# Performance work log

Hardware: AMD Instinct MI355X
Metric: run time of the kernel (lower is better)

Reference implementation:

```python
import jax, jax.numpy as jnp
from jax import lax
import numpy as np

B, H, W, C = 512, 64, 128, 3
FEAT = 13 * 26 * 64  # ceil(64/5)*ceil(128/5)*(32+32) after SAME stride-5 convs + concat


def setup_inputs() -> dict:
    key = jax.random.key(0)
    ks = jax.random.split(key, 6)
    x = jax.random.normal(ks[0], (B, H, W, C), jnp.float32)
    conv0_w = jax.random.normal(ks[1], (3, 3, 3, 32), jnp.float32) * 0.05  # HWIO
    conv1_w = jax.random.normal(ks[2], (5, 5, 3, 32), jnp.float32) * 0.05
    fc0_w = jax.random.normal(ks[3], (FEAT, 32), jnp.float32) * 0.01
    fc0_b = jnp.zeros((32,), jnp.float32)
    fc1_w = jax.random.normal(ks[4], (32, 6), jnp.float32) * 0.1
    fc1_b = jnp.zeros((6,), jnp.float32)
    return {"x": x, "conv0_w": conv0_w, "conv1_w": conv1_w,
            "fc0_w": fc0_w, "fc0_b": fc0_b, "fc1_w": fc1_w, "fc1_b": fc1_b}


def _stn_forward(x, conv0_w, conv1_w, fc0_w, fc0_b, fc1_w, fc1_b):
    b, h, w, c = x.shape
    dn = ("NHWC", "HWIO", "NHWC")
    # ---- LocNet ----
    # AveragePooling2D(3x3, stride 1, SAME); TF avg_pool averages over valid
    # (non-padded) elements only, so normalize by a window-count map.
    psum = lax.reduce_window(x, 0.0, lax.add, (1, 3, 3, 1), (1, 1, 1, 1), "SAME")
    cnt = lax.reduce_window(jnp.ones((1, h, w, 1), x.dtype), 0.0, lax.add,
                            (1, 3, 3, 1), (1, 1, 1, 1), "SAME")
    pooled = psum / cnt
    x0 = jax.nn.relu(lax.conv_general_dilated(pooled, conv0_w, (5, 5), "SAME",
                                              dimension_numbers=dn))
    x1 = jax.nn.relu(lax.conv_general_dilated(x, conv1_w, (5, 5), "SAME",
                                              dimension_numbers=dn))
    feat = jnp.concatenate([x0, x1], axis=-1).reshape(b, -1)
    # Dropout(0.5) is identity at inference.
    hid = jnp.tanh(feat @ fc0_w + fc0_b)
    theta = jnp.tanh(hid @ fc1_w + fc1_b).reshape(b, 2, 3)
    # ---- gen_grid ----
    xt, yt = jnp.meshgrid(jnp.linspace(-1.0, 1.0, w), jnp.linspace(-1.0, 1.0, h))
    grid = jnp.stack([xt.ravel(), yt.ravel(), jnp.ones(h * w, x.dtype)])  # [3, h*w]
    T = jnp.einsum("bij,jk->bik", theta, grid)          # [b, 2, h*w]
    T = T.reshape(b, 2, h, w).transpose(0, 2, 3, 1)     # [b, h, w, 2]
    # ---- grid_sample (bilinear) ----
    gx = (T[..., 0] + 1.0) * w / 2.0
    gy = (T[..., 1] + 1.0) * h / 2.0
    x0f = jnp.clip(jnp.floor(gx), 0.0, w - 2.0)
    x1f = jnp.clip(jnp.floor(gx) + 1.0, 1.0, w - 1.0)
    y0f = jnp.clip(jnp.floor(gy), 0.0, h - 2.0)
    y1f = jnp.clip(jnp.floor(gy) + 1.0, 1.0, h - 1.0)
    xi0, xi1 = x0f.astype(jnp.int32), x1f.astype(jnp.int32)
    yi0, yi1 = y0f.astype(jnp.int32), y1f.astype(jnp.int32)
    bi = jnp.arange(b)[:, None, None]                   # broadcast batch index
    Q00 = x[bi, yi0, xi0]  # [b, h, w, c]
    Q01 = x[bi, yi1, xi0]
    Q10 = x[bi, yi0, xi1]
    Q11 = x[bi, yi1, xi1]
    wx0 = (x1f - gx)[..., None]
    wx1 = (gx - x0f)[..., None]
    wy0 = (y1f - gy)[..., None]
    wy1 = (gy - y0f)[..., None]
    # Wx @ Q @ Wy expanded: rows of Q are x-neighbors, cols are y-neighbors.
    out = wx0 * (wy0 * Q00 + wy1 * Q01) + wx1 * (wy0 * Q10 + wy1 * Q11)
    Wd = ((x1f - x0f) * (y1f - y0f))[..., None]
    return out / Wd


def reference(x, conv0_w, conv1_w, fc0_w, fc0_b, fc1_w, fc1_b):
    return _stn_forward(x, conv0_w, conv1_w, fc0_w, fc0_b, fc1_w, fc1_b)
```

## Files before the change

kernel.cpp:

```cpp
#include <hip/hip_runtime.h>
#include <math.h>

namespace {
constexpr int BN = 512, HH = 64, WW = 128, CC = 3;
constexpr int OHH = 13, OWW = 26;
constexpr int FEATN = OHH * OWW * 64;
constexpr int KCH = 416;
constexpr int NKS = FEATN / KCH;
}

__global__ __launch_bounds__(256, 3) void k_feat(const float* __restrict__ x,
                                                 const float* __restrict__ w0,
                                                 const float* __restrict__ w1,
                                                 float* __restrict__ feat) {
  const int p = blockIdx.x * 256 + threadIdx.x;
  const int b = p / 338;
  const int pos = p - b * 338;
  const int oh = pos / 26;
  const int ow = pos - oh * 26;
  const float* xb = x + (size_t)b * (HH * WW * CC);

  float xv[6][15];
#pragma unroll
  for (int ri = 0; ri < 6; ++ri) {
    const int gr = oh * 5 - 1 + ri;
    const int grc = min(max(gr, 0), HH - 1);
    const bool rv = (gr >= 0) & (gr <= HH - 1);
    const float* rowp = xb + grc * (WW * CC);
#pragma unroll
    for (int pj = 0; pj < 5; ++pj) {
      const int gc = ow * 5 - 1 + pj;
      const int gcc = min(max(gc, 0), WW - 1);
      const bool v = rv & (gc >= 0) & (gc <= WW - 1);
      const float* pp = rowp + gcc * CC;
      const float f0 = pp[0], f1 = pp[1], f2 = pp[2];
      xv[ri][pj * 3 + 0] = v ? f0 : 0.f;
      xv[ri][pj * 3 + 1] = v ? f1 : 0.f;
      xv[ri][pj * 3 + 2] = v ? f2 : 0.f;
    }
  }

  float inv[3][3];
#pragma unroll
  for (int kh = 0; kh < 3; ++kh)
#pragma unroll
    for (int kw = 0; kw < 3; ++kw) {
      const int rc = 3 - ((oh == 0 && kh == 0) ? 1 : 0);
      int cc2 = 3;
      if (ow == 0 && kw == 0) cc2 = 2;
      if (ow == OWW - 1 && kw == 2) cc2 = 2;
      inv[kh][kw] = 1.0f / (float)(rc * cc2);
    }
  float pooled[27];
#pragma unroll
  for (int kh = 0; kh < 3; ++kh)
#pragma unroll
    for (int kw = 0; kw < 3; ++kw)
#pragma unroll
      for (int ic = 0; ic < 3; ++ic) {
        float s = 0.f;
#pragma unroll
        for (int dr = 0; dr < 3; ++dr)
#pragma unroll
          for (int dc = 0; dc < 3; ++dc)
            s += xv[kh + dr][(kw + dc) * 3 + ic];
        pooled[(kh * 3 + kw) * 3 + ic] = s * inv[kh][kw];
      }

  float* fb = feat + (size_t)p * 64;

#pragma unroll 1
  for (int qg = 0; qg < 8; ++qg) {
    float a0 = 0.f, a1 = 0.f, a2 = 0.f, a3 = 0.f;
#pragma unroll
    for (int tap = 0; tap < 27; ++tap) {
      const float pv = pooled[tap];
      const float4 wv = *(const float4*)(w0 + tap * 32 + qg * 4);
      a0 += pv * wv.x; a1 += pv * wv.y; a2 += pv * wv.z; a3 += pv * wv.w;
    }
    fb[qg * 4 + 0] = fmaxf(a0, 0.f);
    fb[qg * 4 + 1] = fmaxf(a1, 0.f);
    fb[qg * 4 + 2] = fmaxf(a2, 0.f);
    fb[qg * 4 + 3] = fmaxf(a3, 0.f);
  }

#pragma unroll 1
  for (int qg = 0; qg < 8; ++qg) {
    float a0 = 0.f, a1 = 0.f, a2 = 0.f, a3 = 0.f;
#pragma unroll
    for (int kh = 0; kh < 5; ++kh)
#pragma unroll
      for (int kw = 0; kw < 5; ++kw)
#pragma unroll
        for (int ic = 0; ic < 3; ++ic) {
          const float pv = xv[kh + 1][kw * 3 + ic];
          const int tap = (kh * 5 + kw) * 3 + ic;
          const float4 wv = *(const float4*)(w1 + tap * 32 + qg * 4);
          a0 += pv * wv.x; a1 += pv * wv.y; a2 += pv * wv.z; a3 += pv * wv.w;
        }
    fb[32 + qg * 4 + 0] = fmaxf(a0, 0.f);
    fb[32 + qg * 4 + 1] = fmaxf(a1, 0.f);
    fb[32 + qg * 4 + 2] = fmaxf(a2, 0.f);
    fb[32 + qg * 4 + 3] = fmaxf(a3, 0.f);
  }
}

__global__ __launch_bounds__(256) void k_fc0(const float* __restrict__ feat,
                                             const float* __restrict__ w,
                                             float* __restrict__ part) {
  const int mt = blockIdx.x / NKS;
  const int ks = blockIdx.x % NKS;
  const int k0 = ks * KCH;
  __shared__ float wsh[KCH * 32];
  const int t = threadIdx.x;
  {
    const float4* wg = (const float4*)(w + (size_t)k0 * 32);
    float4* wl = (float4*)wsh;
    for (int i = t; i < KCH * 8; i += 256) wl[i] = wg[i];
  }
  __syncthreads();
  const int r = t & 63;
  const int og = t >> 6;
  const int m = mt * 64 + r;
  const float* fr = feat + (size_t)m * FEATN + k0;
  float acc[8] = {0.f, 0.f, 0.f, 0.f, 0.f, 0.f, 0.f, 0.f};
  for (int k = 0; k < KCH; k += 4) {
    float4 f = *(const float4*)(fr + k);
    float fv[4] = {f.x, f.y, f.z, f.w};
#pragma unroll
    for (int q = 0; q < 4; ++q) {
      float4 wa = *(const float4*)&wsh[(k + q) * 32 + og * 8];
      float4 wb = *(const float4*)&wsh[(k + q) * 32 + og * 8 + 4];
      acc[0] += fv[q] * wa.x; acc[1] += fv[q] * wa.y;
      acc[2] += fv[q] * wa.z; acc[3] += fv[q] * wa.w;
      acc[4] += fv[q] * wb.x; acc[5] += fv[q] * wb.y;
      acc[6] += fv[q] * wb.z; acc[7] += fv[q] * wb.w;
    }
  }
  float* po = part + ((size_t)ks * 512 + m) * 32 + og * 8;
  *(float4*)po = make_float4(acc[0], acc[1], acc[2], acc[3]);
  *(float4*)(po + 4) = make_float4(acc[4], acc[5], acc[6], acc[7]);
}

__global__ __launch_bounds__(256) void k_theta(const float* __restrict__ part,
                                               const float* __restrict__ b0,
                                               const float* __restrict__ w1,
                                               const float* __restrict__ b1,
                                               float* __restrict__ theta) {
  __shared__ float hid[8][32];
  const int t = threadIdx.x;
  const int bl = t >> 5, oc = t & 31;
  const int bb = blockIdx.x * 8 + bl;
  float s = 0.f;
  for (int ks = 0; ks < NKS; ++ks)
    s += part[(size_t)ks * 512 * 32 + bb * 32 + oc];
  hid[bl][oc] = tanhf(s + b0[oc]);
  __syncthreads();
  if (t < 48) {
    const int bl2 = t / 6, j = t - bl2 * 6;
    float s2 = b1[j];
#pragma unroll
    for (int o2 = 0; o2 < 32; ++o2) s2 += hid[bl2][o2] * w1[o2 * 6 + j];
    theta[(blockIdx.x * 8 + bl2) * 6 + j] = tanhf(s2);
  }
}

__global__ __launch_bounds__(256) void k_sample(const float* __restrict__ x,
                                                const float* __restrict__ theta,
                                                float* __restrict__ out) {
  const int b = blockIdx.x >> 3;
  const int seg = blockIdx.x & 7;
  __shared__ float th[6];
  if (threadIdx.x < 6) th[threadIdx.x] = theta[b * 6 + threadIdx.x];
  __syncthreads();
  const float t00 = th[0], t01 = th[1], t02 = th[2];
  const float t10 = th[3], t11 = th[4], t12 = th[5];
  const int idx = seg * 1024 + threadIdx.x * 4;
  const int i = idx >> 7, j0 = idx & 127;
  const float yt = (float)i * (2.0f / 63.0f) - 1.0f;
  const float* xb = x + (size_t)b * (HH * WW * CC);
  float res[12];
#pragma unroll
  for (int p = 0; p < 4; ++p) {
    const float xt = (float)(j0 + p) * (2.0f / 127.0f) - 1.0f;
    const float gx = (t00 * xt + t01 * yt + t02 + 1.0f) * 64.0f;
    const float gy = (t10 * xt + t11 * yt + t12 + 1.0f) * 32.0f;
    const float fx = floorf(gx), fy = floorf(gy);
    const float x0f = fminf(fmaxf(fx, 0.f), 126.f);
    const float x1f = fminf(fmaxf(fx + 1.f, 1.f), 127.f);
    const float y0f = fminf(fmaxf(fy, 0.f), 62.f);
    const float y1f = fminf(fmaxf(fy + 1.f, 1.f), 63.f);
    const float wx0 = x1f - gx, wx1 = gx - x0f;
    const float wy0 = y1f - gy, wy1 = gy - y0f;
    const int xi0 = (int)x0f, xi1 = (int)x1f;
    const int yi0 = (int)y0f, yi1 = (int)y1f;
    const float* q00 = xb + (yi0 * WW + xi0) * 3;
    const float* q01 = xb + (yi1 * WW + xi0) * 3;
    const float* q10 = xb + (yi0 * WW + xi1) * 3;
    const float* q11 = xb + (yi1 * WW + xi1) * 3;
#pragma unroll
    for (int c = 0; c < 3; ++c)
      res[p * 3 + c] = wx0 * (wy0 * q00[c] + wy1 * q01[c]) +
                       wx1 * (wy0 * q10[c] + wy1 * q11[c]);
  }
  float4* o = (float4*)(out + ((size_t)b * 8192 + idx) * 3);
  o[0] = make_float4(res[0], res[1], res[2], res[3]);
  o[1] = make_float4(res[4], res[5], res[6], res[7]);
  o[2] = make_float4(res[8], res[9], res[10], res[11]);
}

extern "C" void kernel_launch(void* const* d_in, const int* in_sizes, int n_in,
                              void* d_out, int out_size, void* d_ws, size_t ws_size,
                              hipStream_t stream) {
  (void)in_sizes; (void)n_in; (void)out_size; (void)ws_size;
  const float* x   = (const float*)d_in[0];
  const float* w0  = (const float*)d_in[1];
  const float* w1  = (const float*)d_in[2];
  const float* fw0 = (const float*)d_in[3];
  const float* fb0 = (const float*)d_in[4];
  const float* fw1 = (const float*)d_in[5];
  const float* fb1 = (const float*)d_in[6];
  float* outp = (float*)d_out;
  float* feat = outp;
  float* part = outp + (size_t)BN * FEATN;
  float* theta = (float*)d_ws;
  k_feat  <<<(BN * 338) / 256, 256, 0, stream>>>(x, w0, w1, feat);
  k_fc0   <<<8 * NKS, 256, 0, stream>>>(feat, fw0, part);
  k_theta <<<64, 256, 0, stream>>>(part, fb0, fw1, fb1, theta);
  k_sample<<<BN * 8, 256, 0, stream>>>(x, theta, outp);
}
```

Measured before the change: 129.0 us.

## Transpose feature layout to batch-fastest and restructure fc0 as per-row K-split

k_feat now maps threads so batch is the fastest index and writes features into a position-channel-major, batch-contiguous buffer. Stores across a wavefront become contiguous instead of 64-float strided. k_fc0 is rewritten so each thread owns one batch row and accumulates all 32 outputs over a 256-wide K chunk. It reads weights directly from global memory as wavefront-uniform loads instead of staging them in LDS. The risks are less locality for the input loads in k_feat, a small grid of 170 blocks for fc0 on a 256-CU part, and more partial sums for k_theta to reduce.

```diff
diff --git a/kernel.cpp b/kernel.cpp
--- a/kernel.cpp
+++ b/kernel.cpp
@@ -4,18 +4,19 @@
 namespace {
 constexpr int BN = 512, HH = 64, WW = 128, CC = 3;
 constexpr int OHH = 13, OWW = 26;
-constexpr int FEATN = OHH * OWW * 64;
-constexpr int KCH = 416;
-constexpr int NKS = FEATN / KCH;
+constexpr int NPOS = OHH * OWW;
+constexpr int FEATN = NPOS * 64;
+constexpr int KC = 256;
+constexpr int NKS = (FEATN + KC - 1) / KC;
 }
 
 __global__ __launch_bounds__(256, 3) void k_feat(const float* __restrict__ x,
                                                  const float* __restrict__ w0,
                                                  const float* __restrict__ w1,
-                                                 float* __restrict__ feat) {
+                                                 float* __restrict__ featT) {
   const int p = blockIdx.x * 256 + threadIdx.x;
-  const int b = p / 338;
-  const int pos = p - b * 338;
+  const int pos = p >> 9;
+  const int b = p & 511;
   const int oh = pos / 26;
   const int ow = pos - oh * 26;
   const float* xb = x + (size_t)b * (HH * WW * CC);
@@ -67,7 +68,7 @@
         pooled[(kh * 3 + kw) * 3 + ic] = s * inv[kh][kw];
       }
 
-  float* fb = feat + (size_t)p * 64;
+  float* ft = featT + (size_t)pos * 64 * 512 + b;
 
 #pragma unroll 1
   for (int qg = 0; qg < 8; ++qg) {
@@ -78,10 +79,10 @@
       const float4 wv = *(const float4*)(w0 + tap * 32 + qg * 4);
       a0 += pv * wv.x; a1 += pv * wv.y; a2 += pv * wv.z; a3 += pv * wv.w;
     }
-    fb[qg * 4 + 0] = fmaxf(a0, 0.f);
-    fb[qg * 4 + 1] = fmaxf(a1, 0.f);
-    fb[qg * 4 + 2] = fmaxf(a2, 0.f);
-    fb[qg * 4 + 3] = fmaxf(a3, 0.f);
+    ft[(size_t)(qg * 4 + 0) * 512] = fmaxf(a0, 0.f);
+    ft[(size_t)(qg * 4 + 1) * 512] = fmaxf(a1, 0.f);
+    ft[(size_t)(qg * 4 + 2) * 512] = fmaxf(a2, 0.f);
+    ft[(size_t)(qg * 4 + 3) * 512] = fmaxf(a3, 0.f);
   }
 
 #pragma unroll 1
@@ -98,48 +99,38 @@
           const float4 wv = *(const float4*)(w1 + tap * 32 + qg * 4);
           a0 += pv * wv.x; a1 += pv * wv.y; a2 += pv * wv.z; a3 += pv * wv.w;
         }
-    fb[32 + qg * 4 + 0] = fmaxf(a0, 0.f);
-    fb[32 + qg * 4 + 1] = fmaxf(a1, 0.f);
-    fb[32 + qg * 4 + 2] = fmaxf(a2, 0.f);
-    fb[32 + qg * 4 + 3] = fmaxf(a3, 0.f);
-  }
-}
-
-__global__ __launch_bounds__(256) void k_fc0(const float* __restrict__ feat,
+    ft[(size_t)(32 + qg * 4 + 0) * 512] = fmaxf(a0, 0.f);
+    ft[(size_t)(32 + qg * 4 + 1) * 512] = fmaxf(a1, 0.f);
+    ft[(size_t)(32 + qg * 4 + 2) * 512] = fmaxf(a2, 0.f);
+    ft[(size_t)(32 + qg * 4 + 3) * 512] = fmaxf(a3, 0.f);
+  }
+}
+
+__global__ __launch_bounds__(256) void k_fc0(const float* __restrict__ featT,
                                              const float* __restrict__ w,
                                              float* __restrict__ part) {
-  const int mt = blockIdx.x / NKS;
-  const int ks = blockIdx.x % NKS;
-  const int k0 = ks * KCH;
-  __shared__ float wsh[KCH * 32];
-  const int t = threadIdx.x;
-  {
-    const float4* wg = (const float4*)(w + (size_t)k0 * 32);
-    float4* wl = (float4*)wsh;
-    for (int i = t; i < KCH * 8; i += 256) wl[i] = wg[i];
-  }
-  __syncthreads();
-  const int r = t & 63;
-  const int og = t >> 6;
-  const int m = mt * 64 + r;
-  const float* fr = feat + (size_t)m * FEATN + k0;
-  float acc[8] = {0.f, 0.f, 0.f, 0.f, 0.f, 0.f, 0.f, 0.f};
-  for (int k = 0; k < KCH; k += 4) {
-    float4 f = *(const float4*)(fr + k);
-    float fv[4] = {f.x, f.y, f.z, f.w};
-#pragma unroll
-    for (int q = 0; q < 4; ++q) {
-      float4 wa = *(const float4*)&wsh[(k + q) * 32 + og * 8];
-      float4 wb = *(const float4*)&wsh[(k + q) * 32 + og * 8 + 4];
-      acc[0] += fv[q] * wa.x; acc[1] += fv[q] * wa.y;
-      acc[2] += fv[q] * wa.z; acc[3] += fv[q] * wa.w;
-      acc[4] += fv[q] * wb.x; acc[5] += fv[q] * wb.y;
-      acc[6] += fv[q] * wb.z; acc[7] += fv[q] * wb.w;
-    }
-  }
-  float* po = part + ((size_t)ks * 512 + m) * 32 + og * 8;
-  *(float4*)po = make_float4(acc[0], acc[1], acc[2], acc[3]);
-  *(float4*)(po + 4) = make_float4(acc[4], acc[5], acc[6], acc[7]);
+  const int ks = blockIdx.x >> 1;
+  const int mt = blockIdx.x & 1;
+  const int m = mt * 256 + threadIdx.x;
+  const int k0 = ks * KC;
+  const int k1 = min(FEATN, k0 + KC);
+  float acc[32];
+#pragma unroll
+  for (int n = 0; n < 32; ++n) acc[n] = 0.f;
+  for (int kk = k0; kk < k1; ++kk) {
+    const float f = featT[(size_t)kk * 512 + m];
+    const float4* wr = (const float4*)(w + (size_t)kk * 32);
+#pragma unroll
+    for (int q = 0; q < 8; ++q) {
+      const float4 wv = wr[q];
+      acc[q * 4 + 0] += f * wv.x; acc[q * 4 + 1] += f * wv.y;
+      acc[q * 4 + 2] += f * wv.z; acc[q * 4 + 3] += f * wv.w;
+    }
+  }
+  float4* po = (float4*)(part + ((size_t)ks * 512 + m) * 32);
+#pragma unroll
+  for (int q = 0; q < 8; ++q)
+    po[q] = make_float4(acc[q * 4], acc[q * 4 + 1], acc[q * 4 + 2], acc[q * 4 + 3]);
 }
 
 __global__ __launch_bounds__(256) void k_theta(const float* __restrict__ part,
@@ -221,11 +212,11 @@
   const float* fw1 = (const float*)d_in[5];
   const float* fb1 = (const float*)d_in[6];
   float* outp = (float*)d_out;
-  float* feat = outp;
-  float* part = outp + (size_t)BN * FEATN;
+  float* featT = outp;
+  float* part  = outp + (size_t)BN * FEATN;
   float* theta = (float*)d_ws;
-  k_feat  <<<(BN * 338) / 256, 256, 0, stream>>>(x, w0, w1, feat);
-  k_fc0   <<<8 * NKS, 256, 0, stream>>>(feat, fw0, part);
+  k_feat  <<<(BN * NPOS) / 256, 256, 0, stream>>>(x, w0, w1, featT);
+  k_fc0   <<<2 * NKS, 256, 0, stream>>>(featT, fw0, part);
   k_theta <<<64, 256, 0, stream>>>(part, fb0, fw1, fb1, theta);
   k_sample<<<BN * 8, 256, 0, stream>>>(x, theta, outp);
 }
```

After: 167.6 us. 29.9% more time.
